# Performance work log

Measured on AMD Instinct MI355X. Metric: run time of the kernel, lower is better.

The kernel has to match this reference:

```python
import jax, jax.numpy as jnp
import numpy as np

TOPK = 8

def setup_inputs() -> dict:
    key = jax.random.key(0)
    k1, k2, k3, k4 = jax.random.split(key, 4)
    B, T, D = 4, 4096, 1024
    SUB, HALF, VDIM = 512, D // 2, 128
    query = jax.random.normal(k1, (B, T, D), dtype=jnp.float32)
    codebook1 = jax.random.normal(k2, (SUB, HALF), dtype=jnp.float32) * 0.02
    codebook2 = jax.random.normal(k3, (SUB, HALF), dtype=jnp.float32) * 0.02
    values = jax.random.normal(k4, (SUB * SUB, VDIM), dtype=jnp.float32) * 0.02
    return {"query": query, "codebook1": codebook1, "codebook2": codebook2, "values": values}

def reference(query, codebook1, codebook2, values):
    B, T, D = query.shape
    sub_keys, half = codebook1.shape
    q1 = query[..., :half]
    q2 = query[..., half:2 * half]
    # [B,T,sub_keys] score matrices
    s1 = jnp.einsum('btd,kd->btk', q1, codebook1)
    s2 = jnp.einsum('btd,kd->btk', q2, codebook2)
    tk1_vals, tk1_idx = jax.lax.top_k(s1, TOPK)
    tk2_vals, tk2_idx = jax.lax.top_k(s2, TOPK)
    # cartesian combine: [B,T,TOPK,TOPK] -> [B,T,TOPK*TOPK]
    full_idx = (tk1_idx[..., :, None] * sub_keys + tk2_idx[..., None, :]).reshape(B, T, -1)
    w1 = jax.nn.softmax(tk1_vals, axis=-1)
    w2 = jax.nn.softmax(tk2_vals, axis=-1)
    weights = (w1[..., :, None] * w2[..., None, :]).reshape(B, T, -1)
    vals = values[full_idx]  # [B,T,TOPK^2,value_dim] gather
    return jnp.einsum('btk,btkv->btv', weights, vals)
```

## Files before the change

kernel.cpp:

```cpp
#include <hip/hip_runtime.h>
#include <hip/hip_bf16.h>
#include <math.h>

#define NTOK 16384
#define DDIM 1024
#define HALF 512
#define SUB  512
#define KDIM 512
#define TOPK 8
#define NCAND 16
#define VDIM 128
#define TMB 32

typedef __attribute__((ext_vector_type(8))) short bf16x8;
typedef __attribute__((ext_vector_type(4))) float f32x4;

static __device__ __forceinline__ unsigned short f2bf(float x) {
    union { float f; unsigned u; } v; v.f = x;
    unsigned r = v.u + 0x7FFF + ((v.u >> 16) & 1);
    return (unsigned short)(r >> 16);
}

static __device__ __forceinline__ void split_bf(float x, unsigned short& h, unsigned short& l) {
    h = f2bf(x);
    union { unsigned u; float f; } hv; hv.u = ((unsigned)h) << 16;
    l = f2bf(x - hv.f);
}

__global__ __launch_bounds__(256)
void cvt_bfrag(const float* __restrict__ cb1, const float* __restrict__ cb2,
               char* __restrict__ Bp)
{
    int fid  = blockIdx.x * 256 + threadIdx.x;
    int lane = fid & 63;
    int nt   = (fid >> 6) & 7;
    int kc   = (fid >> 9) & 15;
    int cq   = (fid >> 13) & 3;
    int hf   = (fid >> 15) & 1;
    const float* cb = hf ? cb2 : cb1;
    int n  = cq * 128 + nt * 16 + (lane & 15);
    int kb = kc * 32 + (lane >> 4) * 8;
    const float* src = cb + (size_t)n * KDIM + kb;
    float4 f0 = *(const float4*)src;
    float4 f1 = *(const float4*)(src + 4);
    unsigned short hh[8], ll[8];
    split_bf(f0.x, hh[0], ll[0]); split_bf(f0.y, hh[1], ll[1]);
    split_bf(f0.z, hh[2], ll[2]); split_bf(f0.w, hh[3], ll[3]);
    split_bf(f1.x, hh[4], ll[4]); split_bf(f1.y, hh[5], ll[5]);
    split_bf(f1.z, hh[6], ll[6]); split_bf(f1.w, hh[7], ll[7]);
    size_t dst = ((size_t)(hf * 4 + cq) * 128 + (kc * 8 + nt)) * 2048 + lane * 16;
    *(int4*)(Bp + dst)        = *(const int4*)hh;
    *(int4*)(Bp + dst + 1024) = *(const int4*)ll;
}

__global__ __launch_bounds__(256, 2)
void score_topk_mfma(const float* __restrict__ query,
                     const float* __restrict__ cb1f,
                     const float* __restrict__ cb2f,
                     const char* __restrict__ Bp,
                     int*   __restrict__ tk_idx,
                     float* __restrict__ tk_val)
{
    __shared__ char smem[65536];
    char* sAh = smem;
    char* sAl = smem + 32768;
    float* sS = (float*)smem;

    const int tid  = threadIdx.x;
    const int hf   = blockIdx.y;
    const int tok0 = blockIdx.x * TMB;
    const float* __restrict__ cbf = hf ? cb2f : cb1f;
    const int qoff = hf * HALF;

    const int lane = tid & 63;
    const int wid  = tid >> 6;
    const int l15  = lane & 15;
    const int lh   = lane >> 4;
    const int l7   = lane & 7;

    #pragma unroll
    for (int i = 0; i < 8; i++) {
        int c   = i * 256 + tid;
        int row = c >> 6;
        int b8  = c & 63;
        const float* src = query + (size_t)(tok0 + row) * DDIM + qoff + b8 * 8;
        float4 f0 = *(const float4*)(src);
        float4 f1 = *(const float4*)(src + 4);
        unsigned short hh[8], ll[8];
        split_bf(f0.x, hh[0], ll[0]); split_bf(f0.y, hh[1], ll[1]);
        split_bf(f0.z, hh[2], ll[2]); split_bf(f0.w, hh[3], ll[3]);
        split_bf(f1.x, hh[4], ll[4]); split_bf(f1.y, hh[5], ll[5]);
        split_bf(f1.z, hh[6], ll[6]); split_bf(f1.w, hh[7], ll[7]);
        int boff = row * 1024 + ((b8 * 16) ^ ((row & 7) << 4));
        *(int4*)(sAh + boff) = *(const int4*)hh;
        *(int4*)(sAl + boff) = *(const int4*)ll;
    }
    __syncthreads();

    const char* bp = Bp + (size_t)(hf * 4 + wid) * 262144 + lane * 16;

    int4 rh[8], rl[8];
    #pragma unroll
    for (int p = 0; p < 8; p++) {
        rh[p] = *(const int4*)(bp + p * 2048);
        rl[p] = *(const int4*)(bp + p * 2048 + 1024);
    }

    f32x4 acc[2][8];
    #pragma unroll
    for (int tg = 0; tg < 2; tg++)
        #pragma unroll
        for (int nt = 0; nt < 8; nt++) acc[tg][nt] = (f32x4){0.f, 0.f, 0.f, 0.f};

    for (int kc = 0; kc < 16; kc++) {
        const int co = (kc * 64 + lh * 16) ^ (l7 << 4);
        const bf16x8 ah0 = *(const bf16x8*)(sAh + l15 * 1024 + co);
        const bf16x8 al0 = *(const bf16x8*)(sAl + l15 * 1024 + co);
        const bf16x8 ah1 = *(const bf16x8*)(sAh + (16 + l15) * 1024 + co);
        const bf16x8 al1 = *(const bf16x8*)(sAl + (16 + l15) * 1024 + co);
        #pragma unroll
        for (int nt = 0; nt < 8; nt++) {
            union { int4 i; bf16x8 b; } ubh, ubl;
            ubh.i = rh[nt]; ubl.i = rl[nt];
            const int sp = (kc * 8 + nt + 8) & 127;
            rh[nt] = *(const int4*)(bp + sp * 2048);
            rl[nt] = *(const int4*)(bp + sp * 2048 + 1024);
            acc[0][nt] = __builtin_amdgcn_mfma_f32_16x16x32_bf16(ah0, ubh.b, acc[0][nt], 0, 0, 0);
            acc[0][nt] = __builtin_amdgcn_mfma_f32_16x16x32_bf16(al0, ubh.b, acc[0][nt], 0, 0, 0);
            acc[0][nt] = __builtin_amdgcn_mfma_f32_16x16x32_bf16(ah0, ubl.b, acc[0][nt], 0, 0, 0);
            acc[1][nt] = __builtin_amdgcn_mfma_f32_16x16x32_bf16(ah1, ubh.b, acc[1][nt], 0, 0, 0);
            acc[1][nt] = __builtin_amdgcn_mfma_f32_16x16x32_bf16(al1, ubh.b, acc[1][nt], 0, 0, 0);
            acc[1][nt] = __builtin_amdgcn_mfma_f32_16x16x32_bf16(ah1, ubl.b, acc[1][nt], 0, 0, 0);
        }
    }
    __syncthreads();

    #pragma unroll
    for (int tg = 0; tg < 2; tg++)
        #pragma unroll
        for (int nt = 0; nt < 8; nt++)
            #pragma unroll
            for (int r = 0; r < 4; r++) {
                int t = tg * 16 + lh * 4 + r;
                int c = wid * 128 + nt * 16 + l15;
                sS[t * SUB + (c ^ (lh << 3))] = acc[tg][nt][r];
            }
    __syncthreads();

    for (int v = 0; v < 8; v++) {
        const int t   = wid * 8 + v;
        const int tok = tok0 + t;
        const int hsh = ((t >> 2) & 3) << 3;

        float sv[8];
        #pragma unroll
        for (int j = 0; j < 8; j++) sv[j] = sS[t * SUB + ((lane + 64 * j) ^ hsh)];

        float m = sv[0];
        #pragma unroll
        for (int j = 1; j < 8; j++) m = fmaxf(m, sv[j]);
        #pragma unroll
        for (int off = 32; off > 0; off >>= 1) m = fmaxf(m, __shfl_xor(m, off));

        auto wave_cnt = [&](float tau) -> int {
            int c = 0;
            #pragma unroll
            for (int j = 0; j < 8; j++)
                c += __popcll(__ballot(sv[j] > tau));
            return c;
        };

        float lo = m - 0.5f, hi = m;
        while (wave_cnt(lo) < 9) lo -= 0.5f;
        for (int it = 0; it < 14; it++) {
            float mid = 0.5f * (lo + hi);
            if (wave_cnt(mid) >= 9) lo = mid; else hi = mid;
        }
        int ch8 = wave_cnt(hi);

        float v8 = 1e30f, v9 = -1e30f;
        #pragma unroll
        for (int j = 0; j < 8; j++) {
            bool sel = sv[j] > hi;
            v8 = sel ? fminf(v8, sv[j]) : v8;
            v9 = sel ? v9 : fmaxf(v9, sv[j]);
        }
        #pragma unroll
        for (int off = 32; off > 0; off >>= 1) {
            v8 = fminf(v8, __shfl_xor(v8, off));
            v9 = fmaxf(v9, __shfl_xor(v9, off));
        }

        if (ch8 == 8 && (v8 - v9) > 6e-5f) {
            int base = 0;
            #pragma unroll
            for (int j = 0; j < 8; j++) {
                unsigned long long mk = __ballot(sv[j] > hi);
                if (sv[j] > hi) {
                    int pos = base + __popcll(mk & ((1ULL << lane) - 1ULL));
                    tk_idx[((size_t)tok * 2 + hf) * TOPK + pos] = lane + 64 * j;
                    tk_val[((size_t)tok * 2 + hf) * TOPK + pos] = sv[j];
                }
                base += __popcll(mk);
            }
        } else {
            int cand[NCAND];
            #pragma unroll
            for (int r = 0; r < NCAND; r++) {
                float bv = sv[0]; int bj = 0;
                #pragma unroll
                for (int j = 1; j < 8; j++) if (sv[j] > bv) { bv = sv[j]; bj = j; }
                int bidx = lane + 64 * bj;
                #pragma unroll
                for (int off = 32; off > 0; off >>= 1) {
                    float ov = __shfl_xor(bv, off);
                    int   oi = __shfl_xor(bidx, off);
                    if (ov > bv || (ov == bv && oi < bidx)) { bv = ov; bidx = oi; }
                }
                cand[r] = bidx;
                int jj = bidx >> 6;
                if ((bidx & 63) == lane) {
                    #pragma unroll
                    for (int j = 0; j < 8; j++) if (j == jj) sv[j] = -INFINITY;
                }
            }
            double qd[8];
            #pragma unroll
            for (int j = 0; j < 8; j++)
                qd[j] = (double)query[(size_t)tok * DDIM + qoff + lane + 64 * j];
            double rv[NCAND];
            #pragma unroll
            for (int r = 0; r < NCAND; r++) {
                const float* __restrict__ crow = &cbf[(size_t)cand[r] * KDIM];
                double a = 0.0;
                #pragma unroll
                for (int j = 0; j < 8; j++)
                    a = fma(qd[j], (double)crow[lane + 64 * j], a);
                #pragma unroll
                for (int off = 32; off > 0; off >>= 1)
                    a += __shfl_xor(a, off);
                rv[r] = a;
            }
            if (lane == 0) {
                #pragma unroll
                for (int r = 0; r < NCAND; r++) {
                    int rk = 0;
                    #pragma unroll
                    for (int mm = 0; mm < NCAND; mm++)
                        if (rv[mm] > rv[r] || (rv[mm] == rv[r] && cand[mm] < cand[r])) rk++;
                    if (rk < TOPK) {
                        tk_idx[((size_t)tok * 2 + hf) * TOPK + rk] = cand[r];
                        tk_val[((size_t)tok * 2 + hf) * TOPK + rk] = (float)rv[r];
                    }
                }
            }
        }
    }
}

__global__ __launch_bounds__(256)
void gather_kernel(const float* __restrict__ values,
                   const int*   __restrict__ tk_idx,
                   const float* __restrict__ tk_val,
                   float* __restrict__ out)
{
    const int tid  = threadIdx.x;
    const int lane = tid & 63;
    const int tok  = blockIdx.x * 4 + (tid >> 6);

    const int b1 = (tok * 2 + 0) * TOPK;
    const int b2 = (tok * 2 + 1) * TOPK;

    float v1[8], v2[8]; int i1[8], i2[8];
    #pragma unroll
    for (int j = 0; j < 8; j++) {
        i1[j] = tk_idx[b1 + j]; v1[j] = tk_val[b1 + j];
        i2[j] = tk_idx[b2 + j]; v2[j] = tk_val[b2 + j];
    }

    float m1 = v1[0], m2 = v2[0];
    #pragma unroll
    for (int j = 1; j < 8; j++) { m1 = fmaxf(m1, v1[j]); m2 = fmaxf(m2, v2[j]); }

    float w1[8], w2[8], s1 = 0.f, s2 = 0.f;
    #pragma unroll
    for (int j = 0; j < 8; j++) {
        w1[j] = expf(v1[j] - m1); s1 += w1[j];
        w2[j] = expf(v2[j] - m2); s2 += w2[j];
    }
    const float inv1 = 1.f / s1, inv2 = 1.f / s2;
    #pragma unroll
    for (int j = 0; j < 8; j++) { w1[j] *= inv1; w2[j] *= inv2; }

    float2 acc = make_float2(0.f, 0.f);
    #pragma unroll
    for (int i = 0; i < 8; i++) {
        const int rb = i1[i] * SUB;
        const float wi = w1[i];
        #pragma unroll
        for (int j = 0; j < 8; j++) {
            const float w = wi * w2[j];
            const float* __restrict__ row = values + (size_t)(rb + i2[j]) * VDIM;
            float2 tv = *(const float2*)&row[lane * 2];
            acc.x = fmaf(w, tv.x, acc.x);
            acc.y = fmaf(w, tv.y, acc.y);
        }
    }
    *(float2*)&out[(size_t)tok * VDIM + lane * 2] = acc;
}

extern "C" void kernel_launch(void* const* d_in, const int* in_sizes, int n_in,
                              void* d_out, int out_size, void* d_ws, size_t ws_size,
                              hipStream_t stream) {
    const float* query  = (const float*)d_in[0];
    const float* cb1    = (const float*)d_in[1];
    const float* cb2    = (const float*)d_in[2];
    const float* values = (const float*)d_in[3];
    float* out = (float*)d_out;

    char* ws = (char*)d_ws;
    int*   tk_idx = (int*)ws;
    float* tk_val = (float*)(ws + (1u << 20));
    char*  Bp     = ws + (2u << 20);

    cvt_bfrag<<<256, 256, 0, stream>>>(cb1, cb2, Bp);
    dim3 g1(NTOK / TMB, 2);
    score_topk_mfma<<<g1, 256, 0, stream>>>(query, cb1, cb2, Bp, tk_idx, tk_val);
    gather_kernel<<<NTOK / 4, 256, 0, stream>>>(values, tk_idx, tk_val, out);
}
```

Measured before the change: 207.3 us.

## Switch scoring to fp16 split-query MFMA with halved LDS and float4 gather

Scoring moves from a three-term bf16 hi/lo split to fp16. The codebook is stored as a single fp16 term and the query as an fp16 hi/lo pair, so each step issues two MFMAs instead of three and the B fragment stream is halved. The query is staged in two K-halves into 32KB of LDS, which allows three blocks per CU. The top-k pass is split into two 16-token rounds, and the near-tie threshold for falling back to exact recomputation is relaxed from 6e-5 to 1e-3. The gather kernel now reads float4 rows with two half-waves and combines them with a shuffle, at the cost of fp16 codebook rounding error that leans on the fallback path for correctness.

New measurement: 283.1 us. 36.5% more time.

```diff
diff --git a/kernel.cpp b/kernel.cpp
--- a/kernel.cpp
+++ b/kernel.cpp
@@ -12,58 +12,42 @@
 #define VDIM 128
 #define TMB 32
 
-typedef __attribute__((ext_vector_type(8))) short bf16x8;
+typedef __attribute__((ext_vector_type(8))) _Float16 f16x8;
 typedef __attribute__((ext_vector_type(4))) float f32x4;
-
-static __device__ __forceinline__ unsigned short f2bf(float x) {
-    union { float f; unsigned u; } v; v.f = x;
-    unsigned r = v.u + 0x7FFF + ((v.u >> 16) & 1);
-    return (unsigned short)(r >> 16);
-}
-
-static __device__ __forceinline__ void split_bf(float x, unsigned short& h, unsigned short& l) {
-    h = f2bf(x);
-    union { unsigned u; float f; } hv; hv.u = ((unsigned)h) << 16;
-    l = f2bf(x - hv.f);
-}
 
 __global__ __launch_bounds__(256)
 void cvt_bfrag(const float* __restrict__ cb1, const float* __restrict__ cb2,
                char* __restrict__ Bp)
 {
-    int fid  = blockIdx.x * 256 + threadIdx.x;
-    int lane = fid & 63;
-    int nt   = (fid >> 6) & 7;
-    int kc   = (fid >> 9) & 15;
-    int cq   = (fid >> 13) & 3;
-    int hf   = (fid >> 15) & 1;
+    int fid   = blockIdx.x * 256 + threadIdx.x;
+    int lane  = fid & 63;
+    int s     = (fid >> 6) & 127;
+    int slice = fid >> 13;
+    int nt = s & 7, kstep = s >> 3;
+    int cq = slice & 3, hf = slice >> 2;
     const float* cb = hf ? cb2 : cb1;
-    int n  = cq * 128 + nt * 16 + (lane & 15);
-    int kb = kc * 32 + (lane >> 4) * 8;
-    const float* src = cb + (size_t)n * KDIM + kb;
+    int n = cq * 128 + nt * 16 + (lane & 15);
+    int k = kstep * 32 + (lane >> 4) * 8;
+    const float* src = cb + (size_t)n * KDIM + k;
     float4 f0 = *(const float4*)src;
     float4 f1 = *(const float4*)(src + 4);
-    unsigned short hh[8], ll[8];
-    split_bf(f0.x, hh[0], ll[0]); split_bf(f0.y, hh[1], ll[1]);
-    split_bf(f0.z, hh[2], ll[2]); split_bf(f0.w, hh[3], ll[3]);
-    split_bf(f1.x, hh[4], ll[4]); split_bf(f1.y, hh[5], ll[5]);
-    split_bf(f1.z, hh[6], ll[6]); split_bf(f1.w, hh[7], ll[7]);
-    size_t dst = ((size_t)(hf * 4 + cq) * 128 + (kc * 8 + nt)) * 2048 + lane * 16;
-    *(int4*)(Bp + dst)        = *(const int4*)hh;
-    *(int4*)(Bp + dst + 1024) = *(const int4*)ll;
+    union { _Float16 h[8]; int4 v; } u;
+    u.h[0] = (_Float16)f0.x; u.h[1] = (_Float16)f0.y;
+    u.h[2] = (_Float16)f0.z; u.h[3] = (_Float16)f0.w;
+    u.h[4] = (_Float16)f1.x; u.h[5] = (_Float16)f1.y;
+    u.h[6] = (_Float16)f1.z; u.h[7] = (_Float16)f1.w;
+    *(int4*)(Bp + (size_t)fid * 16) = u.v;
 }
 
-__global__ __launch_bounds__(256, 2)
-void score_topk_mfma(const float* __restrict__ query,
-                     const float* __restrict__ cb1f,
-                     const float* __restrict__ cb2f,
-                     const char* __restrict__ Bp,
-                     int*   __restrict__ tk_idx,
-                     float* __restrict__ tk_val)
+__global__ __launch_bounds__(256, 3)
+void score_topk_fused(const float* __restrict__ query,
+                      const float* __restrict__ cb1f,
+                      const float* __restrict__ cb2f,
+                      const char* __restrict__ Bp,
+                      int*   __restrict__ tk_idx,
+                      float* __restrict__ tk_val)
 {
-    __shared__ char smem[65536];
-    char* sAh = smem;
-    char* sAl = smem + 32768;
+    __shared__ char smem[32768];
     float* sS = (float*)smem;
 
     const int tid  = threadIdx.x;
@@ -76,185 +60,196 @@
     const int wid  = tid >> 6;
     const int l15  = lane & 15;
     const int lh   = lane >> 4;
-    const int l7   = lane & 7;
-
-    #pragma unroll
-    for (int i = 0; i < 8; i++) {
-        int c   = i * 256 + tid;
-        int row = c >> 6;
-        int b8  = c & 63;
-        const float* src = query + (size_t)(tok0 + row) * DDIM + qoff + b8 * 8;
-        float4 f0 = *(const float4*)(src);
-        float4 f1 = *(const float4*)(src + 4);
-        unsigned short hh[8], ll[8];
-        split_bf(f0.x, hh[0], ll[0]); split_bf(f0.y, hh[1], ll[1]);
-        split_bf(f0.z, hh[2], ll[2]); split_bf(f0.w, hh[3], ll[3]);
-        split_bf(f1.x, hh[4], ll[4]); split_bf(f1.y, hh[5], ll[5]);
-        split_bf(f1.z, hh[6], ll[6]); split_bf(f1.w, hh[7], ll[7]);
-        int boff = row * 1024 + ((b8 * 16) ^ ((row & 7) << 4));
-        *(int4*)(sAh + boff) = *(const int4*)hh;
-        *(int4*)(sAl + boff) = *(const int4*)ll;
-    }
-    __syncthreads();
-
-    const char* bp = Bp + (size_t)(hf * 4 + wid) * 262144 + lane * 16;
-
-    int4 rh[8], rl[8];
-    #pragma unroll
-    for (int p = 0; p < 8; p++) {
-        rh[p] = *(const int4*)(bp + p * 2048);
-        rl[p] = *(const int4*)(bp + p * 2048 + 1024);
-    }
+
+    const char* bp = Bp + (size_t)(hf * 4 + wid) * 131072 + lane * 16;
+    int4 ring[8];
+    #pragma unroll
+    for (int nt = 0; nt < 8; nt++)
+        ring[nt] = *(const int4*)(bp + nt * 1024);
 
     f32x4 acc[2][8];
     #pragma unroll
-    for (int tg = 0; tg < 2; tg++)
+    for (int tt = 0; tt < 2; tt++)
         #pragma unroll
-        for (int nt = 0; nt < 8; nt++) acc[tg][nt] = (f32x4){0.f, 0.f, 0.f, 0.f};
-
-    for (int kc = 0; kc < 16; kc++) {
-        const int co = (kc * 64 + lh * 16) ^ (l7 << 4);
-        const bf16x8 ah0 = *(const bf16x8*)(sAh + l15 * 1024 + co);
-        const bf16x8 al0 = *(const bf16x8*)(sAl + l15 * 1024 + co);
-        const bf16x8 ah1 = *(const bf16x8*)(sAh + (16 + l15) * 1024 + co);
-        const bf16x8 al1 = *(const bf16x8*)(sAl + (16 + l15) * 1024 + co);
-        #pragma unroll
-        for (int nt = 0; nt < 8; nt++) {
-            union { int4 i; bf16x8 b; } ubh, ubl;
-            ubh.i = rh[nt]; ubl.i = rl[nt];
-            const int sp = (kc * 8 + nt + 8) & 127;
-            rh[nt] = *(const int4*)(bp + sp * 2048);
-            rl[nt] = *(const int4*)(bp + sp * 2048 + 1024);
-            acc[0][nt] = __builtin_amdgcn_mfma_f32_16x16x32_bf16(ah0, ubh.b, acc[0][nt], 0, 0, 0);
-            acc[0][nt] = __builtin_amdgcn_mfma_f32_16x16x32_bf16(al0, ubh.b, acc[0][nt], 0, 0, 0);
-            acc[0][nt] = __builtin_amdgcn_mfma_f32_16x16x32_bf16(ah0, ubl.b, acc[0][nt], 0, 0, 0);
-            acc[1][nt] = __builtin_amdgcn_mfma_f32_16x16x32_bf16(ah1, ubh.b, acc[1][nt], 0, 0, 0);
-            acc[1][nt] = __builtin_amdgcn_mfma_f32_16x16x32_bf16(al1, ubh.b, acc[1][nt], 0, 0, 0);
-            acc[1][nt] = __builtin_amdgcn_mfma_f32_16x16x32_bf16(ah1, ubl.b, acc[1][nt], 0, 0, 0);
+        for (int nt = 0; nt < 8; nt++) acc[tt][nt] = (f32x4){0.f, 0.f, 0.f, 0.f};
+
+    for (int h = 0; h < 2; h++) {
+        {
+            const int tok = tid >> 3;
+            const int seg = tid & 7;
+            const int tt  = tok >> 4;
+            const int row = tok & 15;
+            const float* src = query + (size_t)(tok0 + tok) * DDIM + qoff
+                               + h * 256 + seg * 32;
+            char* base = smem + seg * 4096 + tt * 2048;
+            #pragma unroll
+            for (int j8 = 0; j8 < 4; j8++) {
+                float4 f0 = *(const float4*)(src + j8 * 8);
+                float4 f1 = *(const float4*)(src + j8 * 8 + 4);
+                float x[8] = { f0.x, f0.y, f0.z, f0.w, f1.x, f1.y, f1.z, f1.w };
+                union { _Float16 h[8]; int4 v; } uh, ul;
+                #pragma unroll
+                for (int e = 0; e < 8; e++) {
+                    _Float16 qh = (_Float16)x[e];
+                    uh.h[e] = qh;
+                    ul.h[e] = (_Float16)(x[e] - (float)qh);
+                }
+                const int lw = j8 * 16 + row;
+                *(int4*)(base + lw * 16)        = uh.v;
+                *(int4*)(base + 1024 + lw * 16) = ul.v;
+            }
         }
-    }
-    __syncthreads();
-
-    #pragma unroll
-    for (int tg = 0; tg < 2; tg++)
+        __syncthreads();
+
+        for (int ks = 0; ks < 8; ks++) {
+            f16x8 qh[2], ql[2];
+            #pragma unroll
+            for (int tt = 0; tt < 2; tt++) {
+                qh[tt] = *(const f16x8*)(smem + ks * 4096 + tt * 2048 + lane * 16);
+                ql[tt] = *(const f16x8*)(smem + ks * 4096 + tt * 2048 + 1024 + lane * 16);
+            }
+            const int snext = h * 8 + ks + 1;
+            #pragma unroll
+            for (int np = 0; np < 8; np += 2) {
+                union { int4 i; f16x8 b; } b0, b1;
+                b0.i = ring[np]; b1.i = ring[np + 1];
+                acc[0][np]   = __builtin_amdgcn_mfma_f32_16x16x32_f16(qh[0], b0.b, acc[0][np],   0, 0, 0);
+                acc[1][np]   = __builtin_amdgcn_mfma_f32_16x16x32_f16(qh[1], b0.b, acc[1][np],   0, 0, 0);
+                acc[0][np+1] = __builtin_amdgcn_mfma_f32_16x16x32_f16(qh[0], b1.b, acc[0][np+1], 0, 0, 0);
+                acc[1][np+1] = __builtin_amdgcn_mfma_f32_16x16x32_f16(qh[1], b1.b, acc[1][np+1], 0, 0, 0);
+                ring[np]     = *(const int4*)(bp + ((snext * 8 + np)     & 127) * 1024);
+                ring[np + 1] = *(const int4*)(bp + ((snext * 8 + np + 1) & 127) * 1024);
+                acc[0][np]   = __builtin_amdgcn_mfma_f32_16x16x32_f16(ql[0], b0.b, acc[0][np],   0, 0, 0);
+                acc[1][np]   = __builtin_amdgcn_mfma_f32_16x16x32_f16(ql[1], b0.b, acc[1][np],   0, 0, 0);
+                acc[0][np+1] = __builtin_amdgcn_mfma_f32_16x16x32_f16(ql[0], b1.b, acc[0][np+1], 0, 0, 0);
+                acc[1][np+1] = __builtin_amdgcn_mfma_f32_16x16x32_f16(ql[1], b1.b, acc[1][np+1], 0, 0, 0);
+            }
+        }
+        __syncthreads();
+    }
+
+    #pragma unroll
+    for (int rr = 0; rr < 2; rr++) {
         #pragma unroll
         for (int nt = 0; nt < 8; nt++)
             #pragma unroll
             for (int r = 0; r < 4; r++) {
-                int t = tg * 16 + lh * 4 + r;
+                int t = lh * 4 + r;
                 int c = wid * 128 + nt * 16 + l15;
-                sS[t * SUB + (c ^ (lh << 3))] = acc[tg][nt][r];
-            }
-    __syncthreads();
-
-    for (int v = 0; v < 8; v++) {
-        const int t   = wid * 8 + v;
-        const int tok = tok0 + t;
-        const int hsh = ((t >> 2) & 3) << 3;
-
-        float sv[8];
-        #pragma unroll
-        for (int j = 0; j < 8; j++) sv[j] = sS[t * SUB + ((lane + 64 * j) ^ hsh)];
-
-        float m = sv[0];
-        #pragma unroll
-        for (int j = 1; j < 8; j++) m = fmaxf(m, sv[j]);
-        #pragma unroll
-        for (int off = 32; off > 0; off >>= 1) m = fmaxf(m, __shfl_xor(m, off));
-
-        auto wave_cnt = [&](float tau) -> int {
-            int c = 0;
-            #pragma unroll
-            for (int j = 0; j < 8; j++)
-                c += __popcll(__ballot(sv[j] > tau));
-            return c;
-        };
-
-        float lo = m - 0.5f, hi = m;
-        while (wave_cnt(lo) < 9) lo -= 0.5f;
-        for (int it = 0; it < 14; it++) {
-            float mid = 0.5f * (lo + hi);
-            if (wave_cnt(mid) >= 9) lo = mid; else hi = mid;
+                sS[t * SUB + (c ^ (lh << 3))] = acc[rr][nt][r];
+            }
+        __syncthreads();
+
+        for (int v = 0; v < 4; v++) {
+            const int t   = wid * 4 + v;
+            const int tok = tok0 + rr * 16 + t;
+            const int hsh = ((t >> 2) & 3) << 3;
+
+            float sv[8];
+            #pragma unroll
+            for (int j = 0; j < 8; j++) sv[j] = sS[t * SUB + ((lane + 64 * j) ^ hsh)];
+
+            float m = sv[0];
+            #pragma unroll
+            for (int j = 1; j < 8; j++) m = fmaxf(m, sv[j]);
+            #pragma unroll
+            for (int off = 32; off > 0; off >>= 1) m = fmaxf(m, __shfl_xor(m, off));
+
+            auto wave_cnt = [&](float tau) -> int {
+                int c = 0;
+                #pragma unroll
+                for (int j = 0; j < 8; j++)
+                    c += __popcll(__ballot(sv[j] > tau));
+                return c;
+            };
+
+            float lo = m - 0.5f, hi = m;
+            while (wave_cnt(lo) < 9) lo -= 0.5f;
+            for (int it = 0; it < 14; it++) {
+                float mid = 0.5f * (lo + hi);
+                if (wave_cnt(mid) >= 9) lo = mid; else hi = mid;
+            }
+            int ch8 = wave_cnt(hi);
+
+            float v8 = 1e30f, v9 = -1e30f;
+            #pragma unroll
+            for (int j = 0; j < 8; j++) {
+                bool sel = sv[j] > hi;
+                v8 = sel ? fminf(v8, sv[j]) : v8;
+                v9 = sel ? v9 : fmaxf(v9, sv[j]);
+            }
+            #pragma unroll
+            for (int off = 32; off > 0; off >>= 1) {
+                v8 = fminf(v8, __shfl_xor(v8, off));
+                v9 = fmaxf(v9, __shfl_xor(v9, off));
+            }
+
+            if (ch8 == 8 && (v8 - v9) > 1e-3f) {
+                int base = 0;
+                #pragma unroll
+                for (int j = 0; j < 8; j++) {
+                    unsigned long long mk = __ballot(sv[j] > hi);
+                    if (sv[j] > hi) {
+                        int pos = base + __popcll(mk & ((1ULL << lane) - 1ULL));
+                        tk_idx[((size_t)tok * 2 + hf) * TOPK + pos] = lane + 64 * j;
+                        tk_val[((size_t)tok * 2 + hf) * TOPK + pos] = sv[j];
+                    }
+                    base += __popcll(mk);
+                }
+            } else {
+                int cand[NCAND];
+                #pragma unroll
+                for (int r = 0; r < NCAND; r++) {
+                    float bv = sv[0]; int bj = 0;
+                    #pragma unroll
+                    for (int j = 1; j < 8; j++) if (sv[j] > bv) { bv = sv[j]; bj = j; }
+                    int bidx = lane + 64 * bj;
+                    #pragma unroll
+                    for (int off = 32; off > 0; off >>= 1) {
+                        float ov = __shfl_xor(bv, off);
+                        int   oi = __shfl_xor(bidx, off);
+                        if (ov > bv || (ov == bv && oi < bidx)) { bv = ov; bidx = oi; }
+                    }
+                    cand[r] = bidx;
+                    int jj = bidx >> 6;
+                    if ((bidx & 63) == lane) {
+                        #pragma unroll
+                        for (int j = 0; j < 8; j++) if (j == jj) sv[j] = -INFINITY;
+                    }
+                }
+                double qd[8];
+                #pragma unroll
+                for (int j = 0; j < 8; j++)
+                    qd[j] = (double)query[(size_t)tok * DDIM + qoff + lane + 64 * j];
+                double rv[NCAND];
+                #pragma unroll
+                for (int r = 0; r < NCAND; r++) {
+                    const float* __restrict__ crow = &cbf[(size_t)cand[r] * KDIM];
+                    double a = 0.0;
+                    #pragma unroll
+                    for (int j = 0; j < 8; j++)
+                        a = fma(qd[j], (double)crow[lane + 64 * j], a);
+                    #pragma unroll
+                    for (int off = 32; off > 0; off >>= 1)
+                        a += __shfl_xor(a, off);
+                    rv[r] = a;
+                }
+                if (lane == 0) {
+                    #pragma unroll
+                    for (int r = 0; r < NCAND; r++) {
+                        int rk = 0;
+                        #pragma unroll
+                        for (int mm = 0; mm < NCAND; mm++)
+                            if (rv[mm] > rv[r] || (rv[mm] == rv[r] && cand[mm] < cand[r])) rk++;
+                        if (rk < TOPK) {
+                            tk_idx[((size_t)tok * 2 + hf) * TOPK + rk] = cand[r];
+                            tk_val[((size_t)tok * 2 + hf) * TOPK + rk] = (float)rv[r];
+                        }
+                    }
+                }
+            }
         }
-        int ch8 = wave_cnt(hi);
-
-        float v8 = 1e30f, v9 = -1e30f;
-        #pragma unroll
-        for (int j = 0; j < 8; j++) {
-            bool sel = sv[j] > hi;
-            v8 = sel ? fminf(v8, sv[j]) : v8;
-            v9 = sel ? v9 : fmaxf(v9, sv[j]);
-        }
-        #pragma unroll
-        for (int off = 32; off > 0; off >>= 1) {
-            v8 = fminf(v8, __shfl_xor(v8, off));
-            v9 = fmaxf(v9, __shfl_xor(v9, off));
-        }
-
-        if (ch8 == 8 && (v8 - v9) > 6e-5f) {
-            int base = 0;
-            #pragma unroll
-            for (int j = 0; j < 8; j++) {
-                unsigned long long mk = __ballot(sv[j] > hi);
-                if (sv[j] > hi) {
-                    int pos = base + __popcll(mk & ((1ULL << lane) - 1ULL));
-                    tk_idx[((size_t)tok * 2 + hf) * TOPK + pos] = lane + 64 * j;
-                    tk_val[((size_t)tok * 2 + hf) * TOPK + pos] = sv[j];
-                }
-                base += __popcll(mk);
-            }
-        } else {
-            int cand[NCAND];
-            #pragma unroll
-            for (int r = 0; r < NCAND; r++) {
-                float bv = sv[0]; int bj = 0;
-                #pragma unroll
-                for (int j = 1; j < 8; j++) if (sv[j] > bv) { bv = sv[j]; bj = j; }
-                int bidx = lane + 64 * bj;
-                #pragma unroll
-                for (int off = 32; off > 0; off >>= 1) {
-                    float ov = __shfl_xor(bv, off);
-                    int   oi = __shfl_xor(bidx, off);
-                    if (ov > bv || (ov == bv && oi < bidx)) { bv = ov; bidx = oi; }
-                }
-                cand[r] = bidx;
-                int jj = bidx >> 6;
-                if ((bidx & 63) == lane) {
-                    #pragma unroll
-                    for (int j = 0; j < 8; j++) if (j == jj) sv[j] = -INFINITY;
-                }
-            }
-            double qd[8];
-            #pragma unroll
-            for (int j = 0; j < 8; j++)
-                qd[j] = (double)query[(size_t)tok * DDIM + qoff + lane + 64 * j];
-            double rv[NCAND];
-            #pragma unroll
-            for (int r = 0; r < NCAND; r++) {
-                const float* __restrict__ crow = &cbf[(size_t)cand[r] * KDIM];
-                double a = 0.0;
-                #pragma unroll
-                for (int j = 0; j < 8; j++)
-                    a = fma(qd[j], (double)crow[lane + 64 * j], a);
-                #pragma unroll
-                for (int off = 32; off > 0; off >>= 1)
-                    a += __shfl_xor(a, off);
-                rv[r] = a;
-            }
-            if (lane == 0) {
-                #pragma unroll
-                for (int r = 0; r < NCAND; r++) {
-                    int rk = 0;
-                    #pragma unroll
-                    for (int mm = 0; mm < NCAND; mm++)
-                        if (rv[mm] > rv[r] || (rv[mm] == rv[r] && cand[mm] < cand[r])) rk++;
-                    if (rk < TOPK) {
-                        tk_idx[((size_t)tok * 2 + hf) * TOPK + rk] = cand[r];
-                        tk_val[((size_t)tok * 2 + hf) * TOPK + rk] = (float)rv[r];
-                    }
-                }
-            }
-        }
+        __syncthreads();
     }
 }
 
@@ -292,21 +287,32 @@
     #pragma unroll
     for (int j = 0; j < 8; j++) { w1[j] *= inv1; w2[j] *= inv2; }
 
-    float2 acc = make_float2(0.f, 0.f);
-    #pragma unroll
-    for (int i = 0; i < 8; i++) {
-        const int rb = i1[i] * SUB;
-        const float wi = w1[i];
-        #pragma unroll
-        for (int j = 0; j < 8; j++) {
-            const float w = wi * w2[j];
-            const float* __restrict__ row = values + (size_t)(rb + i2[j]) * VDIM;
-            float2 tv = *(const float2*)&row[lane * 2];
-            acc.x = fmaf(w, tv.x, acc.x);
-            acc.y = fmaf(w, tv.y, acc.y);
-        }
-    }
-    *(float2*)&out[(size_t)tok * VDIM + lane * 2] = acc;
+    const int hi  = lane >> 5;
+    const int col = lane & 31;
+    const float4* vbase = (const float4*)values;
+
+    float4 a0 = {0.f, 0.f, 0.f, 0.f}, a1 = {0.f, 0.f, 0.f, 0.f};
+    #pragma unroll
+    for (int p = 0; p < 32; p += 2) {
+        const int ia = p >> 2,       ja = ((p & 3) << 1) | hi;
+        const int ib = (p + 1) >> 2, jb = (((p + 1) & 3) << 1) | hi;
+        float4 ra = vbase[(size_t)(i1[ia] * SUB + i2[ja]) * 32 + col];
+        float4 rb = vbase[(size_t)(i1[ib] * SUB + i2[jb]) * 32 + col];
+        const float wa = w1[ia] * w2[ja];
+        const float wb = w1[ib] * w2[jb];
+        a0.x = fmaf(wa, ra.x, a0.x); a0.y = fmaf(wa, ra.y, a0.y);
+        a0.z = fmaf(wa, ra.z, a0.z); a0.w = fmaf(wa, ra.w, a0.w);
+        a1.x = fmaf(wb, rb.x, a1.x); a1.y = fmaf(wb, rb.y, a1.y);
+        a1.z = fmaf(wb, rb.z, a1.z); a1.w = fmaf(wb, rb.w, a1.w);
+    }
+    float4 s;
+    s.x = a0.x + a1.x; s.y = a0.y + a1.y; s.z = a0.z + a1.z; s.w = a0.w + a1.w;
+    s.x += __shfl_xor(s.x, 32);
+    s.y += __shfl_xor(s.y, 32);
+    s.z += __shfl_xor(s.z, 32);
+    s.w += __shfl_xor(s.w, 32);
+    if (hi == 0)
+        *(float4*)(out + (size_t)tok * VDIM + col * 4) = s;
 }
 
 extern "C" void kernel_launch(void* const* d_in, const int* in_sizes, int n_in,
@@ -325,6 +331,6 @@
 
     cvt_bfrag<<<256, 256, 0, stream>>>(cb1, cb2, Bp);
     dim3 g1(NTOK / TMB, 2);
-    score_topk_mfma<<<g1, 256, 0, stream>>>(query, cb1, cb2, Bp, tk_idx, tk_val);
+    score_topk_fused<<<g1, 256, 0, stream>>>(query, cb1, cb2, Bp, tk_idx, tk_val);
     gather_kernel<<<NTOK / 4, 256, 0, stream>>>(values, tk_idx, tk_val, out);
 }
```
